# Performance work log

Measured on AMD Instinct MI355X. Metric: run time of the kernel, lower is better.

The kernel has to match this reference:

```python
import jax, jax.numpy as jnp
import numpy as np

N_NODES = 50000
N_EDGES = 500000
IN_DIM = 128
OUT_DIM = 128
T_DIM = 1
NUM_ROUTING = 3
NUM_PERSP = 4
BETA = -1.0
EPSILON = 1e-12
ACOSH_MIN = 1.0 + 1e-6
CLIP_VAL = 10000.0
MAX_TANH_VAL = 10.0


def _inner(x, y):
    # pseudo-Riemannian inner product, time dims negated; keepdims
    return (-jnp.sum(x[..., :T_DIM] * y[..., :T_DIM], axis=-1, keepdims=True)
            + jnp.sum(x[..., T_DIM:] * y[..., T_DIM:], axis=-1, keepdims=True))


def _log_map(x, ref):
    x = jnp.clip(x, -CLIP_VAL, CLIP_VAL)
    inner = _inner(x, ref)
    ref_sq = _inner(ref, ref)
    x_sq = _inner(x, x)
    denom = jnp.sqrt(jnp.clip(jnp.abs(ref_sq * x_sq), EPSILON, None))
    cos_dist = jnp.clip(-inner / denom, ACOSH_MIN, None)
    dist = jnp.arccosh(cos_dist)
    sin_dist = jnp.clip(jnp.sqrt(cos_dist ** 2 - 1.0), EPSILON, None)
    coef = dist / sin_dist
    return coef * (x + (inner / ref_sq) * ref)


def _exp_map(v, ref):
    v_norm = jnp.clip(jnp.sqrt(jnp.abs(_inner(v, v)) + EPSILON), None, MAX_TANH_VAL)
    return jnp.cosh(v_norm) * ref + (jnp.sinh(v_norm) / v_norm) * v


def _squash(s):
    norm_sq = jnp.sum(s ** 2, axis=-1, keepdims=True)
    scale = norm_sq / (1.0 + norm_sq)
    return scale * (s / jnp.sqrt(norm_sq + 1e-9))


def setup_inputs() -> dict:
    key = jax.random.key(0)
    ks = jax.random.split(key, 7)
    x = jax.random.normal(ks[0], (N_NODES, IN_DIM), dtype=jnp.float32)
    edge_index = jax.random.randint(ks[1], (2, N_EDGES), 0, N_NODES, dtype=jnp.int32)
    lim1 = 1.0 / np.sqrt(IN_DIM)
    W_per = jax.random.uniform(ks[2], (IN_DIM, OUT_DIM * NUM_PERSP), jnp.float32, -lim1, lim1)
    b_per = jax.random.uniform(ks[3], (OUT_DIM * NUM_PERSP,), jnp.float32, -lim1, lim1)
    W_gate = jax.random.uniform(ks[4], (IN_DIM, NUM_PERSP), jnp.float32, -lim1, lim1)
    b_gate = jax.random.uniform(ks[5], (NUM_PERSP,), jnp.float32, -lim1, lim1)
    bias = jnp.zeros((1, OUT_DIM), dtype=jnp.float32)
    return {"x": x, "edge_index": edge_index, "W_per": W_per, "b_per": b_per,
            "W_gate": W_gate, "b_gate": b_gate, "bias": bias}


def reference(x, edge_index, W_per, b_per, W_gate, b_gate, bias):
    N = x.shape[0]
    row, col = edge_index[0], edge_index[1]
    # pole: beta=-1 -> sqrt(|beta|) in time slot 0
    ref = jnp.zeros((1, x.shape[1]), x.dtype).at[0, 0].set(np.sqrt(abs(BETA)))
    x_tangent = _log_map(x, ref)              # dropout is identity in eval mode
    xc = x_tangent[row]                        # [E, in_dim]
    u_k = (xc @ W_per + b_per).reshape(-1, NUM_PERSP, OUT_DIM)
    gate = jax.nn.softmax(xc @ W_gate + b_gate, axis=-1)[..., None]
    u_hat = jnp.sum(u_k * gate, axis=1)        # [E, out_dim]
    u_b = u_hat + bias
    b_ij = jnp.zeros(row.shape[0], x.dtype)
    s_j = jnp.zeros((N, OUT_DIM), x.dtype)
    for r in range(NUM_ROUTING):
        m = jax.ops.segment_max(b_ij, col, num_segments=N)
        e = jnp.exp(b_ij - m[col])
        z = jax.ops.segment_sum(e, col, num_segments=N)
        c_ij = e / z[col]                      # scatter_softmax over col
        s_j = jax.ops.segment_sum(c_ij[:, None] * u_b, col, num_segments=N)
        s_j = _squash(s_j)
        if r < NUM_ROUTING - 1:
            b_ij = b_ij + jnp.sum(s_j[col] * u_hat, axis=-1)
    return _exp_map(s_j, ref)
```

## Files before the change

kernel.cpp:

```cpp
#include <hip/hip_runtime.h>
#include <hip/hip_fp16.h>
#include <hip/hip_bf16.h>

typedef short bf16x8 __attribute__((ext_vector_type(8)));
typedef float f32x4 __attribute__((ext_vector_type(4)));
typedef _Float16 f16x2 __attribute__((ext_vector_type(2)));

#define LGKM_FENCE() asm volatile("s_waitcnt lgkmcnt(0)" ::: "memory")
#define CAP 32

static __device__ __forceinline__ f16x2 as_f16x2(uint v) {
  union { uint u; f16x2 h; } c; c.u = v; return c.h;
}

static __device__ __forceinline__ float dot2acc(uint a, uint b, float c) {
#if __has_builtin(__builtin_amdgcn_fdot2)
  return __builtin_amdgcn_fdot2(as_f16x2(a), as_f16x2(b), c, false);
#else
  float2 af = __half22float2(*(const __half2*)&a);
  float2 bf = __half22float2(*(const __half2*)&b);
  return fmaf(af.x, bf.x, fmaf(af.y, bf.y, c));
#endif
}

__global__ __launch_bounds__(256) void k_tangent_gate(
    const float* __restrict__ x, const float* __restrict__ Wg,
    const float* __restrict__ bg, __hip_bfloat16* __restrict__ xtb,
    float* __restrict__ gate, const float* __restrict__ Wp,
    __hip_bfloat16* __restrict__ Wt, int* __restrict__ zbase,
    int nz, int N) {
  int tb = (N + 3) >> 2;
  if ((int)blockIdx.x >= tb + 256) {
    int idx = (blockIdx.x - tb - 256) * 256 + threadIdx.x;
    if (idx < nz) zbase[idx] = 0;
    return;
  }
  if ((int)blockIdx.x >= tb) {
    int idx = (blockIdx.x - tb) * 256 + threadIdx.x;
    if (idx < 512 * 128) {
      int n = idx >> 7, k = idx & 127;
      Wt[idx] = __float2bfloat16(Wp[(size_t)k * 512 + n]);
    }
    return;
  }
  int wid = (blockIdx.x * blockDim.x + threadIdx.x) >> 6;
  int lane = threadIdx.x & 63;
  if (wid >= N) return;

  const float* xr = x + (size_t)wid * 128;
  float2 xv = *(const float2*)(xr + lane * 2);
  xv.x = fminf(fmaxf(xv.x, -10000.f), 10000.f);
  xv.y = fminf(fmaxf(xv.y, -10000.f), 10000.f);

  float p = xv.x * xv.x + xv.y * xv.y;
  if (lane == 0) p -= 2.f * xv.x * xv.x;
  #pragma unroll
  for (int s = 32; s; s >>= 1) p += __shfl_xor(p, s);
  float x0 = __shfl(xv.x, 0);

  float denom = sqrtf(fmaxf(fabsf(p), 1e-12f));
  float cosd = fmaxf(x0 / denom, 1.0f + 1e-6f);
  float t = cosd - 1.0f;
  float coef = (t < 1e-3f)
      ? 1.0f - t * (1.f / 3.f) + t * t * (2.f / 15.f)
      : acoshf(cosd) * rsqrtf(t * (2.f + t));

  float2 o;
  o.x = coef * ((lane == 0) ? 2.0f * xv.x : xv.x);
  o.y = coef * xv.y;
  __hip_bfloat162 hb = __float22bfloat162_rn(make_float2(o.x, o.y));
  *(__hip_bfloat162*)(xtb + (size_t)wid * 128 + lane * 2) = hb;

  const float4 w0 = *(const float4*)(Wg + (size_t)(lane * 2) * 4);
  const float4 w1 = *(const float4*)(Wg + (size_t)(lane * 2 + 1) * 4);
  float g0 = o.x * w0.x + o.y * w1.x;
  float g1 = o.x * w0.y + o.y * w1.y;
  float g2 = o.x * w0.z + o.y * w1.z;
  float g3 = o.x * w0.w + o.y * w1.w;
  #pragma unroll
  for (int s = 32; s; s >>= 1) {
    g0 += __shfl_xor(g0, s); g1 += __shfl_xor(g1, s);
    g2 += __shfl_xor(g2, s); g3 += __shfl_xor(g3, s);
  }
  g0 += bg[0]; g1 += bg[1]; g2 += bg[2]; g3 += bg[3];
  float m = fmaxf(fmaxf(g0, g1), fmaxf(g2, g3));
  float e0 = expf(g0 - m), e1 = expf(g1 - m), e2 = expf(g2 - m), e3 = expf(g3 - m);
  float z = e0 + e1 + e2 + e3;
  if (lane == 0)
    *(float4*)(gate + (size_t)wid * 4) = make_float4(e0 / z, e1 / z, e2 / z, e3 / z);
}

#define TPB 4
__global__ __launch_bounds__(256, 2) void k_uhat_mfma(
    const short* __restrict__ xtb, const float* __restrict__ gate,
    const short* __restrict__ Wt, const float* __restrict__ bp,
    __half* __restrict__ uh, const int* __restrict__ row,
    const int* __restrict__ col, int* __restrict__ cnt,
    int* __restrict__ slots, int* __restrict__ ovf_cnt,
    int2* __restrict__ ovf, int N, int ntiles, int E) {
  int ub = (ntiles + TPB - 1) / TPB;
  if ((int)blockIdx.x >= ub) {
    int e0 = ((blockIdx.x - ub) * 256 + threadIdx.x) * 2;
    #pragma unroll
    for (int k = 0; k < 2; ++k) {
      int e = e0 + k;
      if (e < E) {
        int c = col[e];
        int p = atomicAdd(&cnt[c], 1);
        if (p < CAP) slots[(size_t)c * CAP + p] = row[e];
        else { int q = atomicAdd(ovf_cnt, 1); ovf[q] = make_int2(c, row[e]); }
      }
    }
    return;
  }

  int lane = threadIdx.x & 63;
  int wv = threadIdx.x >> 6;
  int ri = lane & 15, kg = lane >> 4;
  int c_lo = wv * 32;

  bf16x8 bfr[4][2][4];
  float bpv[4][2];
  #pragma unroll
  for (int p = 0; p < 4; ++p)
    #pragma unroll
    for (int n2 = 0; n2 < 2; ++n2) {
      int bcol = p * 128 + c_lo + n2 * 16 + ri;
      #pragma unroll
      for (int ks = 0; ks < 4; ++ks)
        bfr[p][n2][ks] = *(const bf16x8*)(Wt + (((size_t)bcol) << 7) + ks * 32 + kg * 8);
      bpv[p][n2] = bp[bcol];
    }

  int t0 = blockIdx.x * TPB;

  bf16x8 af[TPB][4];
  #pragma unroll
  for (int tt = 0; tt < TPB; ++tt) {
    int t = t0 + tt;
    int r0 = t * 16 + ri;
    int c0 = (t < ntiles) ? ((r0 < N) ? r0 : (N - 1)) : 0;
    #pragma unroll
    for (int ks = 0; ks < 4; ++ks)
      af[tt][ks] = *(const bf16x8*)(xtb + (((size_t)c0) << 7) + ks * 32 + kg * 8);
  }

  #pragma unroll
  for (int tt = 0; tt < TPB; ++tt) {
    int t = t0 + tt;
    if (t < ntiles) {
      int m0 = t * 16;
      int rb = m0 + kg * 4;
      float gg[4][4];
      #pragma unroll
      for (int q = 0; q < 4; ++q) {
        int rm = rb + q;
        bool ok = rm < N;
        float4 gv = *(const float4*)(gate + (size_t)(ok ? rm : 0) * 4);
        gg[q][0] = ok ? gv.x : 0.f;
        gg[q][1] = ok ? gv.y : 0.f;
        gg[q][2] = ok ? gv.z : 0.f;
        gg[q][3] = ok ? gv.w : 0.f;
      }

      float fin[2][4];
      #pragma unroll
      for (int n2 = 0; n2 < 2; ++n2)
        #pragma unroll
        for (int q = 0; q < 4; ++q) fin[n2][q] = 0.f;

      #pragma unroll
      for (int p = 0; p < 4; ++p)
        #pragma unroll
        for (int n2 = 0; n2 < 2; ++n2) {
          f32x4 acc = {0.f, 0.f, 0.f, 0.f};
          #pragma unroll
          for (int ks = 0; ks < 4; ++ks)
            acc = __builtin_amdgcn_mfma_f32_16x16x32_bf16(af[tt][ks], bfr[p][n2][ks], acc, 0, 0, 0);
          #pragma unroll
          for (int q = 0; q < 4; ++q)
            fin[n2][q] += gg[q][p] * (acc[q] + bpv[p][n2]);
        }

      #pragma unroll
      for (int n2 = 0; n2 < 2; ++n2) {
        int cn = c_lo + n2 * 16 + ri;
        #pragma unroll
        for (int q = 0; q < 4; ++q) {
          int rm = rb + q;
          if (rm < N) uh[(size_t)rm * 128 + cn] = __float2half_rn(fin[n2][q]);
        }
      }
    }
  }
}

__global__ __launch_bounds__(64, 4) void k_route(
    const __half* __restrict__ uh, const float* __restrict__ bias,
    const int* __restrict__ cnt, const int* __restrict__ slots,
    const int* __restrict__ ovf_cnt, const int2* __restrict__ ovf,
    int* __restrict__ fbc, int* __restrict__ claim,
    int* __restrict__ fb_rows, float* __restrict__ fb_b,
    float* __restrict__ out, int N) {
  __shared__ __align__(16) uint ssw[64];
  int lane = threadIdx.x;
  int j = blockIdx.x;
  int deg = cnt[j];
  int d0 = lane * 2;

  if (deg == 0) {
    *(float2*)(out + (size_t)j * 128 + d0) =
        make_float2((lane == 0) ? 1.f : 0.f, 0.f);
    return;
  }

  float2 bia = *(const float2*)(bias + d0);
  float s0 = 0.f, s1 = 0.f;
  const uint* uhw = (const uint*)uh;

  if (deg <= 8) {
    int myrow = (lane < deg) ? slots[(size_t)j * CAP + lane] : 0;

    int e = lane >> 3, o = lane & 7;
    int er = __shfl(myrow, (e < deg) ? e : 0);
    const uint4* up = (const uint4*)(uhw + (((size_t)(uint)er) << 6) + o * 8);
    uint4 ud8[2];
    ud8[0] = up[0]; ud8[1] = up[1];

    uint g[8];
    #pragma unroll
    for (int k = 0; k < 8; ++k) {
      int rr = __builtin_amdgcn_readlane(myrow, k);
      uint v = uhw[(((size_t)(uint)rr) << 6) + lane];
      g[k] = (k < deg) ? v : 0u;
    }

    float2 uf[8];
    float a0 = 0.f, a1 = 0.f;
    #pragma unroll
    for (int k = 0; k < 8; ++k) {
      uf[k] = __half22float2(*(const __half2*)&g[k]);
      a0 += uf[k].x; a1 += uf[k].y;
    }

    float invd = 1.f / (float)deg;
    s0 = a0 * invd + bia.x;
    s1 = a1 * invd + bia.y;
    {
      float ns = s0 * s0 + s1 * s1;
      #pragma unroll
      for (int s = 32; s; s >>= 1) ns += __shfl_xor(ns, s);
      float scale = (ns / (1.f + ns)) * rsqrtf(ns + 1e-9f);
      s0 *= scale; s1 *= scale;
    }

    const uint* ssw_o = &ssw[o * 8];
    bool act = (e < deg);
    float b = 0.f;

    #pragma unroll
    for (int r = 0; r < 2; ++r) {
      __half2 sh2 = __floats2half2_rn(s0, s1);
      ssw[lane] = *(const uint*)&sh2;
      LGKM_FENCE();

      float acc0 = 0.f, acc1 = 0.f;
      #pragma unroll
      for (int w4 = 0; w4 < 2; ++w4) {
        uint4 sw = *(const uint4*)&ssw_o[w4 * 4];
        acc0 = dot2acc(ud8[w4].x, sw.x, acc0);
        acc1 = dot2acc(ud8[w4].y, sw.y, acc1);
        acc0 = dot2acc(ud8[w4].z, sw.z, acc0);
        acc1 = dot2acc(ud8[w4].w, sw.w, acc1);
      }
      float acc = acc0 + acc1;
      acc += __shfl_xor(acc, 1);
      acc += __shfl_xor(acc, 2);
      acc += __shfl_xor(acc, 4);
      b += acc;
      float eb = act ? __expf(b) : 0.f;

      float z0 = 0.f, z1 = 0.f, wa0 = 0.f, wa1 = 0.f, wb0 = 0.f, wb1 = 0.f;
      #pragma unroll
      for (int k = 0; k < 8; ++k) {
        float ev = __uint_as_float(
            __builtin_amdgcn_readlane(__float_as_uint(eb), 8 * k));
        if (k & 1) { z1 += ev; wa1 = fmaf(ev, uf[k].x, wa1); wb1 = fmaf(ev, uf[k].y, wb1); }
        else       { z0 += ev; wa0 = fmaf(ev, uf[k].x, wa0); wb0 = fmaf(ev, uf[k].y, wb0); }
      }
      float z = z0 + z1;
      float invz = 1.f / z;
      s0 = (wa0 + wa1) * invz + bia.x;
      s1 = (wb0 + wb1) * invz + bia.y;
      float ns = s0 * s0 + s1 * s1;
      #pragma unroll
      for (int s = 32; s; s >>= 1) ns += __shfl_xor(ns, s);
      float scale = (ns / (1.f + ns)) * rsqrtf(ns + 1e-9f);
      s0 *= scale; s1 *= scale;
    }
  } else if (deg <= 16) {
    int myrow = (lane < deg) ? slots[(size_t)j * CAP + lane] : 0;

    int e = lane >> 2, q = lane & 3;
    int er = __shfl(myrow, (e < deg) ? e : 0);
    const uint4* up = (const uint4*)(uhw + (((size_t)(uint)er) << 6) + q * 16);
    uint4 ud4[4];
    #pragma unroll
    for (int w4 = 0; w4 < 4; ++w4) ud4[w4] = up[w4];

    uint g[16];
    #pragma unroll
    for (int c = 0; c < 16; c += 8) {
      if (c < deg) {
        #pragma unroll
        for (int k = 0; k < 8; ++k) {
          int i = c + k;
          int rr = __builtin_amdgcn_readlane(myrow, i);
          uint v = uhw[(((size_t)(uint)rr) << 6) + lane];
          g[i] = (i < deg) ? v : 0u;
        }
      }
    }

    float2 uf[16];
    float a0 = 0.f, a1 = 0.f;
    #pragma unroll
    for (int c = 0; c < 16; c += 8) {
      if (c < deg) {
        #pragma unroll
        for (int k = 0; k < 8; ++k) {
          int i = c + k;
          uf[i] = __half22float2(*(const __half2*)&g[i]);
          a0 += uf[i].x; a1 += uf[i].y;
        }
      }
    }

    float invd = 1.f / (float)deg;
    s0 = a0 * invd + bia.x;
    s1 = a1 * invd + bia.y;
    {
      float ns = s0 * s0 + s1 * s1;
      #pragma unroll
      for (int s = 32; s; s >>= 1) ns += __shfl_xor(ns, s);
      float scale = (ns / (1.f + ns)) * rsqrtf(ns + 1e-9f);
      s0 *= scale; s1 *= scale;
    }

    const uint* ssw_q = &ssw[q * 16];
    bool act = (e < deg);
    float b = 0.f;

    #pragma unroll
    for (int r = 0; r < 2; ++r) {
      __half2 sh2 = __floats2half2_rn(s0, s1);
      ssw[lane] = *(const uint*)&sh2;
      LGKM_FENCE();

      float acc0 = 0.f, acc1 = 0.f;
      #pragma unroll
      for (int w4 = 0; w4 < 4; ++w4) {
        uint4 sw = *(const uint4*)&ssw_q[w4 * 4];
        acc0 = dot2acc(ud4[w4].x, sw.x, acc0);
        acc1 = dot2acc(ud4[w4].y, sw.y, acc1);
        acc0 = dot2acc(ud4[w4].z, sw.z, acc0);
        acc1 = dot2acc(ud4[w4].w, sw.w, acc1);
      }
      float acc = acc0 + acc1;
      acc += __shfl_xor(acc, 1);
      acc += __shfl_xor(acc, 2);
      b += acc;
      float eb = act ? __expf(b) : 0.f;

      float z0 = 0.f, z1 = 0.f, wa0 = 0.f, wa1 = 0.f, wb0 = 0.f, wb1 = 0.f;
      #pragma unroll
      for (int c = 0; c < 16; c += 8) {
        if (c < deg) {
          #pragma unroll
          for (int k = 0; k < 8; ++k) {
            int i = c + k;
            float ev = __uint_as_float(
                __builtin_amdgcn_readlane(__float_as_uint(eb), 4 * i));
            if (k & 1) { z1 += ev; wa1 = fmaf(ev, uf[i].x, wa1); wb1 = fmaf(ev, uf[i].y, wb1); }
            else       { z0 += ev; wa0 = fmaf(ev, uf[i].x, wa0); wb0 = fmaf(ev, uf[i].y, wb0); }
          }
        }
      }
      float z = z0 + z1;
      float invz = 1.f / z;
      s0 = (wa0 + wa1) * invz + bia.x;
      s1 = (wb0 + wb1) * invz + bia.y;
      float ns = s0 * s0 + s1 * s1;
      #pragma unroll
      for (int s = 32; s; s >>= 1) ns += __shfl_xor(ns, s);
      float scale = (ns / (1.f + ns)) * rsqrtf(ns + 1e-9f);
      s0 *= scale; s1 *= scale;
    }
  } else if (deg <= CAP) {
    int myrow = (lane < deg) ? slots[(size_t)j * CAP + lane] : 0;

    int e = lane >> 1, h = lane & 1;
    int er = __shfl(myrow, (e < deg) ? e : 0);
    const uint4* up = (const uint4*)(uhw + (((size_t)(uint)er) << 6) + h * 32);
    uint4 ud[8];
    #pragma unroll
    for (int k4 = 0; k4 < 8; ++k4) ud[k4] = up[k4];

    uint g[CAP];
    #pragma unroll
    for (int c = 0; c < CAP; c += 8) {
      if (c < deg) {
        #pragma unroll
        for (int k = 0; k < 8; ++k) {
          int i = c + k;
          int rr = __builtin_amdgcn_readlane(myrow, i);
          uint v = uhw[(((size_t)(uint)rr) << 6) + lane];
          g[i] = (i < deg) ? v : 0u;
        }
      }
    }

    float a0 = 0.f, a1 = 0.f;
    #pragma unroll
    for (int c = 0; c < CAP; c += 8) {
      if (c < deg) {
        #pragma unroll
        for (int k = 0; k < 8; ++k) {
          int i = c + k;
          float2 uf = __half22float2(*(const __half2*)&g[i]);
          a0 += uf.x; a1 += uf.y;
        }
      }
    }

    float invd = 1.f / (float)deg;
    s0 = a0 * invd + bia.x;
    s1 = a1 * invd + bia.y;
    {
      float ns = s0 * s0 + s1 * s1;
      #pragma unroll
      for (int s = 32; s; s >>= 1) ns += __shfl_xor(ns, s);
      float scale = (ns / (1.f + ns)) * rsqrtf(ns + 1e-9f);
      s0 *= scale; s1 *= scale;
    }

    const uint* ssw_h = &ssw[h * 32];
    bool act = (e < deg);
    float b = 0.f;

    #pragma unroll
    for (int r = 0; r < 2; ++r) {
      __half2 sh2 = __floats2half2_rn(s0, s1);
      ssw[lane] = *(const uint*)&sh2;
      LGKM_FENCE();

      float acc0 = 0.f, acc1 = 0.f;
      #pragma unroll
      for (int k4 = 0; k4 < 8; ++k4) {
        uint4 sw = *(const uint4*)&ssw_h[k4 * 4];
        acc0 = dot2acc(ud[k4].x, sw.x, acc0);
        acc1 = dot2acc(ud[k4].y, sw.y, acc1);
        acc0 = dot2acc(ud[k4].z, sw.z, acc0);
        acc1 = dot2acc(ud[k4].w, sw.w, acc1);
      }
      float acc = acc0 + acc1;
      acc += __shfl_xor(acc, 1);
      b += acc;
      float eb = act ? __expf(b) : 0.f;

      float z0 = 0.f, z1 = 0.f, wa0 = 0.f, wa1 = 0.f, wb0 = 0.f, wb1 = 0.f;
      #pragma unroll
      for (int c = 0; c < CAP; c += 8) {
        if (c < deg) {
          #pragma unroll
          for (int k = 0; k < 8; ++k) {
            int i = c + k;
            float ev = __uint_as_float(
                __builtin_amdgcn_readlane(__float_as_uint(eb), 2 * i));
            float2 uf = __half22float2(*(const __half2*)&g[i]);
            if (k & 1) { z1 += ev; wa1 = fmaf(ev, uf.x, wa1); wb1 = fmaf(ev, uf.y, wb1); }
            else       { z0 += ev; wa0 = fmaf(ev, uf.x, wa0); wb0 = fmaf(ev, uf.y, wb0); }
          }
        }
      }
      float z = z0 + z1;
      float invz = 1.f / z;
      s0 = (wa0 + wa1) * invz + bia.x;
      s1 = (wb0 + wb1) * invz + bia.y;
      float ns = s0 * s0 + s1 * s1;
      #pragma unroll
      for (int s = 32; s; s >>= 1) ns += __shfl_xor(ns, s);
      float scale = (ns / (1.f + ns)) * rsqrtf(ns + 1e-9f);
      s0 *= scale; s1 *= scale;
    }
  } else {
    int base = 0;
    if (lane == 0) base = atomicAdd(claim, deg);
    base = __shfl(base, 0);
    int* mr = fb_rows + base;
    float* b = fb_b + base;
    if (lane < CAP) mr[lane] = slots[(size_t)j * CAP + lane];
    int novf = *ovf_cnt;
    for (int t = lane; t < novf; t += 64) {
      int2 ov = ovf[t];
      if (ov.x == j) {
        int p = atomicAdd(&fbc[j], 1);
        mr[CAP + p] = ov.y;
      }
    }
    asm volatile("s_waitcnt vmcnt(0)" ::: "memory");

    const __half2* uh2 = (const __half2*)uh;
    for (int i = lane; i < deg; i += 64) atomicExch(&b[i], 0.f);
    asm volatile("s_waitcnt vmcnt(0)" ::: "memory");

    for (int r = 0; r < 3; ++r) {
      float mx = -3.4e38f;
      for (int i = lane; i < deg; i += 64)
        mx = fmaxf(mx, atomicAdd(&b[i], 0.f));
      #pragma unroll
      for (int s = 32; s; s >>= 1) mx = fmaxf(mx, __shfl_xor(mx, s));
      float z = 0.f;
      for (int i = lane; i < deg; i += 64) z += expf(atomicAdd(&b[i], 0.f) - mx);
      #pragma unroll
      for (int s = 32; s; s >>= 1) z += __shfl_xor(z, s);
      float invz = 1.f / z;

      s0 = 0.f; s1 = 0.f;
      for (int i = 0; i < deg; ++i) {
        float c = expf(atomicAdd(&b[i], 0.f) - mx) * invz;
        int rr = mr[i];
        float2 uf = __half22float2(uh2[(((size_t)rr) << 6) + lane]);
        s0 = fmaf(c, uf.x, s0);
        s1 = fmaf(c, uf.y, s1);
      }
      s0 += bia.x; s1 += bia.y;

      float ns = s0 * s0 + s1 * s1;
      #pragma unroll
      for (int s = 32; s; s >>= 1) ns += __shfl_xor(ns, s);
      float scale = (ns / (1.f + ns)) * rsqrtf(ns + 1e-9f);
      s0 *= scale; s1 *= scale;

      if (r < 2) {
        for (int i = 0; i < deg; ++i) {
          int rr = mr[i];
          float2 uf = __half22float2(uh2[(((size_t)rr) << 6) + lane]);
          float pp = s0 * uf.x + s1 * uf.y;
          #pragma unroll
          for (int s = 32; s; s >>= 1) pp += __shfl_xor(pp, s);
          if (lane == 0) atomicAdd(&b[i], pp);
        }
        asm volatile("s_waitcnt vmcnt(0)" ::: "memory");
      }
    }
  }

  float pn = s0 * s0 + s1 * s1;
  if (lane == 0) pn -= 2.f * s0 * s0;
  #pragma unroll
  for (int s = 32; s; s >>= 1) pn += __shfl_xor(pn, s);
  float vn = fminf(sqrtf(fabsf(pn) + 1e-12f), 10.f);
  float sh = sinhf(vn) / vn;
  float ov0 = sh * s0 + ((lane == 0) ? coshf(vn) : 0.f);
  float ov1 = sh * s1;
  *(float2*)(out + (size_t)j * 128 + d0) = make_float2(ov0, ov1);
}

extern "C" void kernel_launch(void* const* d_in, const int* in_sizes, int n_in,
                              void* d_out, int out_size, void* d_ws, size_t ws_size,
                              hipStream_t stream) {
  const float* x    = (const float*)d_in[0];
  const int*   ei   = (const int*)d_in[1];
  const float* Wp   = (const float*)d_in[2];
  const float* bp   = (const float*)d_in[3];
  const float* Wg   = (const float*)d_in[4];
  const float* bg   = (const float*)d_in[5];
  const float* bias = (const float*)d_in[6];
  float* out = (float*)d_out;

  int N = in_sizes[0] / 128;
  int E = in_sizes[1] / 2;
  const int* row = ei;
  const int* col = ei + E;

  __hip_bfloat16* xtb = (__hip_bfloat16*)d_ws;
  __half* uhh = (__half*)(xtb + (size_t)N * 128);
  float* gate = (float*)(uhh + (size_t)N * 128);
  __hip_bfloat16* Wt = (__hip_bfloat16*)(gate + (size_t)N * 4);
  int* cnt = (int*)(Wt + 512 * 128);
  int* fbc = cnt + N;
  int* claim = fbc + N;
  int* ovf_cnt = claim + 1;
  int* slots = ovf_cnt + 1;
  int2* ovf = (int2*)(slots + (size_t)N * CAP);
  int* fb_rows = (int*)(ovf + E);
  float* fb_b = (float*)(fb_rows + E);

  int tb = (N + 3) / 4;
  int hb = (E + 511) / 512;
  int nz = 2 * N + 2;
  int zb = (nz + 255) / 256;
  int ntiles = (N + 15) / 16;
  int ub = (ntiles + TPB - 1) / TPB;
  k_tangent_gate<<<tb + 256 + zb, 256, 0, stream>>>(
      x, Wg, bg, xtb, gate, Wp, Wt, cnt, nz, N);
  k_uhat_mfma<<<ub + hb, 256, 0, stream>>>(
      (const short*)xtb, gate, (const short*)Wt, bp, uhh,
      row, col, cnt, slots, ovf_cnt, ovf, N, ntiles, E);
  k_route<<<N, 64, 0, stream>>>(
      uhh, bias, cnt, slots, ovf_cnt, ovf, fbc, claim, fb_rows, fb_b, out, N);
}
```

Measured before the change: 126.9 us.

## Fuse tangent log-map and gate softmax into MFMA u_hat kernel via LDS

The per-node log-map and gate softmax are now computed inside the MFMA projection kernel. Each block stages its 64 rows of bf16 tangent vectors and gate weights in shared memory instead of writing them to global memory and reading them back. The weight transpose and counter zeroing move into a small separate kernel. This removes the global round trip for xtb and gate. The cost is that each block runs a serial 16-row-per-wave prologue before its MFMA work, and the larger LDS footprint may limit occupancy.

```diff
diff --git a/kernel.cpp b/kernel.cpp
--- a/kernel.cpp
+++ b/kernel.cpp
@@ -23,82 +23,28 @@
 #endif
 }
 
-__global__ __launch_bounds__(256) void k_tangent_gate(
-    const float* __restrict__ x, const float* __restrict__ Wg,
-    const float* __restrict__ bg, __hip_bfloat16* __restrict__ xtb,
-    float* __restrict__ gate, const float* __restrict__ Wp,
-    __hip_bfloat16* __restrict__ Wt, int* __restrict__ zbase,
-    int nz, int N) {
-  int tb = (N + 3) >> 2;
-  if ((int)blockIdx.x >= tb + 256) {
-    int idx = (blockIdx.x - tb - 256) * 256 + threadIdx.x;
+__global__ __launch_bounds__(256) void k_wt(
+    const float* __restrict__ Wp, __hip_bfloat16* __restrict__ Wt,
+    int* __restrict__ zbase, int nz) {
+  if ((int)blockIdx.x >= 256) {
+    int idx = (blockIdx.x - 256) * 256 + threadIdx.x;
     if (idx < nz) zbase[idx] = 0;
     return;
   }
-  if ((int)blockIdx.x >= tb) {
-    int idx = (blockIdx.x - tb) * 256 + threadIdx.x;
-    if (idx < 512 * 128) {
-      int n = idx >> 7, k = idx & 127;
-      Wt[idx] = __float2bfloat16(Wp[(size_t)k * 512 + n]);
-    }
-    return;
-  }
-  int wid = (blockIdx.x * blockDim.x + threadIdx.x) >> 6;
-  int lane = threadIdx.x & 63;
-  if (wid >= N) return;
-
-  const float* xr = x + (size_t)wid * 128;
-  float2 xv = *(const float2*)(xr + lane * 2);
-  xv.x = fminf(fmaxf(xv.x, -10000.f), 10000.f);
-  xv.y = fminf(fmaxf(xv.y, -10000.f), 10000.f);
-
-  float p = xv.x * xv.x + xv.y * xv.y;
-  if (lane == 0) p -= 2.f * xv.x * xv.x;
-  #pragma unroll
-  for (int s = 32; s; s >>= 1) p += __shfl_xor(p, s);
-  float x0 = __shfl(xv.x, 0);
-
-  float denom = sqrtf(fmaxf(fabsf(p), 1e-12f));
-  float cosd = fmaxf(x0 / denom, 1.0f + 1e-6f);
-  float t = cosd - 1.0f;
-  float coef = (t < 1e-3f)
-      ? 1.0f - t * (1.f / 3.f) + t * t * (2.f / 15.f)
-      : acoshf(cosd) * rsqrtf(t * (2.f + t));
-
-  float2 o;
-  o.x = coef * ((lane == 0) ? 2.0f * xv.x : xv.x);
-  o.y = coef * xv.y;
-  __hip_bfloat162 hb = __float22bfloat162_rn(make_float2(o.x, o.y));
-  *(__hip_bfloat162*)(xtb + (size_t)wid * 128 + lane * 2) = hb;
-
-  const float4 w0 = *(const float4*)(Wg + (size_t)(lane * 2) * 4);
-  const float4 w1 = *(const float4*)(Wg + (size_t)(lane * 2 + 1) * 4);
-  float g0 = o.x * w0.x + o.y * w1.x;
-  float g1 = o.x * w0.y + o.y * w1.y;
-  float g2 = o.x * w0.z + o.y * w1.z;
-  float g3 = o.x * w0.w + o.y * w1.w;
-  #pragma unroll
-  for (int s = 32; s; s >>= 1) {
-    g0 += __shfl_xor(g0, s); g1 += __shfl_xor(g1, s);
-    g2 += __shfl_xor(g2, s); g3 += __shfl_xor(g3, s);
-  }
-  g0 += bg[0]; g1 += bg[1]; g2 += bg[2]; g3 += bg[3];
-  float m = fmaxf(fmaxf(g0, g1), fmaxf(g2, g3));
-  float e0 = expf(g0 - m), e1 = expf(g1 - m), e2 = expf(g2 - m), e3 = expf(g3 - m);
-  float z = e0 + e1 + e2 + e3;
-  if (lane == 0)
-    *(float4*)(gate + (size_t)wid * 4) = make_float4(e0 / z, e1 / z, e2 / z, e3 / z);
+  int idx = blockIdx.x * 256 + threadIdx.x;
+  int n = idx >> 7, k = idx & 127;
+  Wt[idx] = __float2bfloat16(Wp[(size_t)k * 512 + n]);
 }
 
-#define TPB 4
-__global__ __launch_bounds__(256, 2) void k_uhat_mfma(
-    const short* __restrict__ xtb, const float* __restrict__ gate,
-    const short* __restrict__ Wt, const float* __restrict__ bp,
-    __half* __restrict__ uh, const int* __restrict__ row,
-    const int* __restrict__ col, int* __restrict__ cnt,
-    int* __restrict__ slots, int* __restrict__ ovf_cnt,
-    int2* __restrict__ ovf, int N, int ntiles, int E) {
-  int ub = (ntiles + TPB - 1) / TPB;
+__global__ __launch_bounds__(256, 2) void k_front(
+    const float* __restrict__ x, const float* __restrict__ Wg,
+    const float* __restrict__ bg, const short* __restrict__ Wt,
+    const float* __restrict__ bp, __half* __restrict__ uh,
+    const int* __restrict__ row, const int* __restrict__ col,
+    int* __restrict__ cnt, int* __restrict__ slots,
+    int* __restrict__ ovf_cnt, int2* __restrict__ ovf,
+    int N, int ntiles, int E) {
+  int ub = (ntiles + 3) / 4;
   if ((int)blockIdx.x >= ub) {
     int e0 = ((blockIdx.x - ub) * 256 + threadIdx.x) * 2;
     #pragma unroll
@@ -114,8 +60,68 @@
     return;
   }
 
+  __shared__ short sA[64][136];
+  __shared__ float sg[64][4];
+
   int lane = threadIdx.x & 63;
   int wv = threadIdx.x >> 6;
+  int m0 = blockIdx.x * 64;
+
+  const float4 w0 = *(const float4*)(Wg + (size_t)(lane * 2) * 4);
+  const float4 w1 = *(const float4*)(Wg + (size_t)(lane * 2 + 1) * 4);
+  float bg0 = bg[0], bg1 = bg[1], bg2 = bg[2], bg3 = bg[3];
+
+  for (int rr = 0; rr < 16; ++rr) {
+    int lr = wv * 16 + rr;
+    int r = m0 + lr;
+    bool ok = r < N;
+    const float* xr = x + (size_t)(ok ? r : 0) * 128;
+    float2 xv = *(const float2*)(xr + lane * 2);
+    xv.x = fminf(fmaxf(xv.x, -10000.f), 10000.f);
+    xv.y = fminf(fmaxf(xv.y, -10000.f), 10000.f);
+
+    float p = xv.x * xv.x + xv.y * xv.y;
+    if (lane == 0) p -= 2.f * xv.x * xv.x;
+    #pragma unroll
+    for (int s = 32; s; s >>= 1) p += __shfl_xor(p, s);
+    float x0 = __shfl(xv.x, 0);
+
+    float denom = sqrtf(fmaxf(fabsf(p), 1e-12f));
+    float cosd = fmaxf(x0 / denom, 1.0f + 1e-6f);
+    float t = cosd - 1.0f;
+    float coef = (t < 1e-3f)
+        ? 1.0f - t * (1.f / 3.f) + t * t * (2.f / 15.f)
+        : acoshf(cosd) * rsqrtf(t * (2.f + t));
+
+    float2 o;
+    o.x = coef * ((lane == 0) ? 2.0f * xv.x : xv.x);
+    o.y = coef * xv.y;
+    if (!ok) { o.x = 0.f; o.y = 0.f; }
+    __hip_bfloat162 hb = __float22bfloat162_rn(make_float2(o.x, o.y));
+    *(__hip_bfloat162*)(&sA[lr][lane * 2]) = hb;
+
+    float g0 = o.x * w0.x + o.y * w1.x;
+    float g1 = o.x * w0.y + o.y * w1.y;
+    float g2 = o.x * w0.z + o.y * w1.z;
+    float g3 = o.x * w0.w + o.y * w1.w;
+    #pragma unroll
+    for (int s = 32; s; s >>= 1) {
+      g0 += __shfl_xor(g0, s); g1 += __shfl_xor(g1, s);
+      g2 += __shfl_xor(g2, s); g3 += __shfl_xor(g3, s);
+    }
+    if (lane == 0) {
+      g0 += bg0; g1 += bg1; g2 += bg2; g3 += bg3;
+      float m = fmaxf(fmaxf(g0, g1), fmaxf(g2, g3));
+      float e0 = expf(g0 - m), e1 = expf(g1 - m);
+      float e2 = expf(g2 - m), e3 = expf(g3 - m);
+      float z = e0 + e1 + e2 + e3;
+      float4 gv = ok ? make_float4(e0 / z, e1 / z, e2 / z, e3 / z)
+                     : make_float4(0.f, 0.f, 0.f, 0.f);
+      *(float4*)(&sg[lr][0]) = gv;
+    }
+  }
+  __syncthreads();
+
   int ri = lane & 15, kg = lane >> 4;
   int c_lo = wv * 32;
 
@@ -132,35 +138,23 @@
       bpv[p][n2] = bp[bcol];
     }
 
-  int t0 = blockIdx.x * TPB;
-
-  bf16x8 af[TPB][4];
+  int t0 = blockIdx.x * 4;
   #pragma unroll
-  for (int tt = 0; tt < TPB; ++tt) {
-    int t = t0 + tt;
-    int r0 = t * 16 + ri;
-    int c0 = (t < ntiles) ? ((r0 < N) ? r0 : (N - 1)) : 0;
-    #pragma unroll
-    for (int ks = 0; ks < 4; ++ks)
-      af[tt][ks] = *(const bf16x8*)(xtb + (((size_t)c0) << 7) + ks * 32 + kg * 8);
-  }
-
-  #pragma unroll
-  for (int tt = 0; tt < TPB; ++tt) {
+  for (int tt = 0; tt < 4; ++tt) {
     int t = t0 + tt;
     if (t < ntiles) {
-      int m0 = t * 16;
-      int rb = m0 + kg * 4;
+      bf16x8 af[4];
+      #pragma unroll
+      for (int ks = 0; ks < 4; ++ks)
+        af[ks] = *(const bf16x8*)(&sA[tt * 16 + ri][ks * 32 + kg * 8]);
+
+      int rb = t * 16 + kg * 4;
+      int lb = tt * 16 + kg * 4;
       float gg[4][4];
       #pragma unroll
       for (int q = 0; q < 4; ++q) {
-        int rm = rb + q;
-        bool ok = rm < N;
-        float4 gv = *(const float4*)(gate + (size_t)(ok ? rm : 0) * 4);
-        gg[q][0] = ok ? gv.x : 0.f;
-        gg[q][1] = ok ? gv.y : 0.f;
-        gg[q][2] = ok ? gv.z : 0.f;
-        gg[q][3] = ok ? gv.w : 0.f;
+        float4 gv = *(const float4*)(&sg[lb + q][0]);
+        gg[q][0] = gv.x; gg[q][1] = gv.y; gg[q][2] = gv.z; gg[q][3] = gv.w;
       }
 
       float fin[2][4];
@@ -176,7 +170,7 @@
           f32x4 acc = {0.f, 0.f, 0.f, 0.f};
           #pragma unroll
           for (int ks = 0; ks < 4; ++ks)
-            acc = __builtin_amdgcn_mfma_f32_16x16x32_bf16(af[tt][ks], bfr[p][n2][ks], acc, 0, 0, 0);
+            acc = __builtin_amdgcn_mfma_f32_16x16x32_bf16(af[ks], bfr[p][n2][ks], acc, 0, 0, 0);
           #pragma unroll
           for (int q = 0; q < 4; ++q)
             fin[n2][q] += gg[q][p] * (acc[q] + bpv[p][n2]);
@@ -584,10 +578,8 @@
   const int* row = ei;
   const int* col = ei + E;
 
-  __hip_bfloat16* xtb = (__hip_bfloat16*)d_ws;
-  __half* uhh = (__half*)(xtb + (size_t)N * 128);
-  float* gate = (float*)(uhh + (size_t)N * 128);
-  __hip_bfloat16* Wt = (__hip_bfloat16*)(gate + (size_t)N * 4);
+  __half* uhh = (__half*)d_ws;
+  __hip_bfloat16* Wt = (__hip_bfloat16*)(uhh + (size_t)N * 128);
   int* cnt = (int*)(Wt + 512 * 128);
   int* fbc = cnt + N;
   int* claim = fbc + N;
@@ -597,16 +589,14 @@
   int* fb_rows = (int*)(ovf + E);
   float* fb_b = (float*)(fb_rows + E);
 
-  int tb = (N + 3) / 4;
   int hb = (E + 511) / 512;
   int nz = 2 * N + 2;
   int zb = (nz + 255) / 256;
   int ntiles = (N + 15) / 16;
-  int ub = (ntiles + TPB - 1) / TPB;
-  k_tangent_gate<<<tb + 256 + zb, 256, 0, stream>>>(
-      x, Wg, bg, xtb, gate, Wp, Wt, cnt, nz, N);
-  k_uhat_mfma<<<ub + hb, 256, 0, stream>>>(
-      (const short*)xtb, gate, (const short*)Wt, bp, uhh,
+  int ub = (ntiles + 3) / 4;
+  k_wt<<<256 + zb, 256, 0, stream>>>(Wp, Wt, cnt, nz);
+  k_front<<<ub + hb, 256, 0, stream>>>(
+      x, Wg, bg, (const short*)Wt, bp, uhh,
       row, col, cnt, slots, ovf_cnt, ovf, N, ntiles, E);
   k_route<<<N, 64, 0, stream>>>(
       uhh, bias, cnt, slots, ovf_cnt, ovf, fbc, claim, fb_rows, fb_b, out, N);
```

New measurement: 129.4 us. About the same (+2.0%).
